# Kernel optimization log

Hardware: AMD Instinct MI355X
Metric: run time of the kernel (lower is better)

The kernel has to match this reference:

```python
import jax, jax.numpy as jnp
import numpy as np

# Output order of the stacked loss vector (7,):
# [loss_pose_intra_t, loss_pose_inter_t, loss_pose_intra_s, loss_pose_inter_s,
#  loss_pose_t, loss_pose_s, loss_pose]
ALPHA_T = 0.5
ALPHA_S = 0.75
ALPHA_TS = 0.5
EPS = 1e-8


def setup_inputs() -> dict:
    key = jax.random.key(0)
    k1, k2 = jax.random.split(key)
    B, M, C = 32, 784, 4
    pred_dT = jax.random.normal(k1, (B, M, M, C), dtype=jnp.float32)
    gt_dT = jax.random.normal(k2, (B, M, M, C), dtype=jnp.float32)
    # V=4 views, 196 tokens each; sum(Ms) must equal M
    Ms = jnp.full((4,), 196, dtype=jnp.int32)
    return {"pred_dT": pred_dT, "gt_dT": gt_dT, "Ms": Ms}


def reference(pred_dT, gt_dT, Ms):
    B, M, _, C = pred_dT.shape
    V = Ms.shape[0]
    dtype = pred_dT.dtype

    # criterion = 'mse', reduction='none'
    loss_full = (pred_dT - gt_dT) ** 2  # (B, M, M, C)

    # view id per token; same-view (intra) pair mask (M, M)
    view_ids = jnp.repeat(jnp.arange(V), Ms, total_repeat_length=M)
    intra_mask = (view_ids[:, None] == view_ids[None, :]).astype(dtype)

    # per-channel sums over all pairs and over intra-view pairs
    per_ch_all = loss_full.sum(axis=(0, 1, 2))                       # (C,)
    per_ch_intra = jnp.einsum('bijc,ij->c', loss_full, intra_mask)   # (C,)

    total_all_t = per_ch_all[0:2].sum()
    total_all_s = per_ch_all[2:4].sum()
    total_intra_t = per_ch_intra[0:2].sum()
    total_intra_s = per_ch_intra[2:4].sum()
    total_inter_t = total_all_t - total_intra_t
    total_inter_s = total_all_s - total_intra_s

    sum_Ms_sq = jnp.sum(Ms * Ms)
    diag_count = (sum_Ms_sq * B).astype(dtype)
    offdiag_count = ((M * M - sum_Ms_sq) * B).astype(dtype)

    zero = jnp.zeros((), dtype)
    loss_intra_t = jnp.where(diag_count > EPS, total_intra_t / diag_count, zero)
    loss_inter_t = jnp.where(offdiag_count > EPS, total_inter_t / offdiag_count, zero)
    loss_intra_s = jnp.where(diag_count > EPS, total_intra_s / diag_count, zero)
    loss_inter_s = jnp.where(offdiag_count > EPS, total_inter_s / offdiag_count, zero)

    loss_t = ALPHA_T * loss_inter_t + (1.0 - ALPHA_T) * loss_intra_t
    loss_s = ALPHA_S * loss_inter_s + (1.0 - ALPHA_S) * loss_intra_s
    loss = ALPHA_TS * loss_t + (1.0 - ALPHA_TS) * loss_s

    return jnp.stack([loss_intra_t, loss_inter_t, loss_intra_s, loss_inter_s,
                      loss_t, loss_s, loss])
```

## Files before the change

kernel.cpp:

```cpp
#include <hip/hip_runtime.h>

constexpr int B_ = 32;
constexpr int M_ = 784;
constexpr int C_ = 4;

constexpr int NBLK = 2048;
constexpr int NTHR = 256;

constexpr float ALPHA_T  = 0.5f;
constexpr float ALPHA_S  = 0.75f;
constexpr float ALPHA_TS = 0.5f;
constexpr float EPS      = 1e-8f;

__global__ __launch_bounds__(NTHR) void pose_loss_partial_kernel(
    const float* __restrict__ pred, const float* __restrict__ gt,
    const int* __restrict__ Ms, float4* __restrict__ partials)
{
    const int cum0 = Ms[0];
    const int cum1 = cum0 + Ms[1];
    const int cum2 = cum1 + Ms[2];

    float all_t = 0.f, all_s = 0.f, intra_t = 0.f, intra_s = 0.f;

    const int R = B_ * M_;
    for (int row = blockIdx.x; row < R; row += gridDim.x) {
        const int i  = row % M_;
        const int vi = (i >= cum0) + (i >= cum1) + (i >= cum2);
        const float4* __restrict__ prow =
            reinterpret_cast<const float4*>(pred + (size_t)row * (M_ * C_));
        const float4* __restrict__ grow =
            reinterpret_cast<const float4*>(gt   + (size_t)row * (M_ * C_));
        for (int j = threadIdx.x; j < M_; j += NTHR) {
            const float4 p = prow[j];
            const float4 g = grow[j];
            const float d0 = p.x - g.x;
            const float d1 = p.y - g.y;
            const float d2 = p.z - g.z;
            const float d3 = p.w - g.w;
            const float t = d0 * d0 + d1 * d1;
            const float s = d2 * d2 + d3 * d3;
            all_t += t;
            all_s += s;
            const int vj = (j >= cum0) + (j >= cum1) + (j >= cum2);
            if (vi == vj) { intra_t += t; intra_s += s; }
        }
    }

    float v0 = all_t, v1 = all_s, v2 = intra_t, v3 = intra_s;
    #pragma unroll
    for (int off = 32; off > 0; off >>= 1) {
        v0 += __shfl_down(v0, off, 64);
        v1 += __shfl_down(v1, off, 64);
        v2 += __shfl_down(v2, off, 64);
        v3 += __shfl_down(v3, off, 64);
    }

    __shared__ float4 sm[NTHR / 64];
    const int lane = threadIdx.x & 63;
    const int wid  = threadIdx.x >> 6;
    if (lane == 0) sm[wid] = make_float4(v0, v1, v2, v3);
    __syncthreads();

    if (threadIdx.x == 0) {
        float4 acc = sm[0];
        #pragma unroll
        for (int w = 1; w < NTHR / 64; ++w) {
            acc.x += sm[w].x; acc.y += sm[w].y;
            acc.z += sm[w].z; acc.w += sm[w].w;
        }
        partials[blockIdx.x] = acc;
    }
}

__global__ __launch_bounds__(NTHR) void pose_loss_final_kernel(
    const float4* __restrict__ partials, const int* __restrict__ Ms,
    float* __restrict__ out)
{
    float v0 = 0.f, v1 = 0.f, v2 = 0.f, v3 = 0.f;
    for (int p = threadIdx.x; p < NBLK; p += NTHR) {
        const float4 q = partials[p];
        v0 += q.x; v1 += q.y; v2 += q.z; v3 += q.w;
    }
    #pragma unroll
    for (int off = 32; off > 0; off >>= 1) {
        v0 += __shfl_down(v0, off, 64);
        v1 += __shfl_down(v1, off, 64);
        v2 += __shfl_down(v2, off, 64);
        v3 += __shfl_down(v3, off, 64);
    }
    __shared__ float4 sm[NTHR / 64];
    const int lane = threadIdx.x & 63;
    const int wid  = threadIdx.x >> 6;
    if (lane == 0) sm[wid] = make_float4(v0, v1, v2, v3);
    __syncthreads();

    if (threadIdx.x == 0) {
        float4 acc = sm[0];
        #pragma unroll
        for (int w = 1; w < NTHR / 64; ++w) {
            acc.x += sm[w].x; acc.y += sm[w].y;
            acc.z += sm[w].z; acc.w += sm[w].w;
        }
        const float total_all_t   = acc.x;
        const float total_all_s   = acc.y;
        const float total_intra_t = acc.z;
        const float total_intra_s = acc.w;
        const float total_inter_t = total_all_t - total_intra_t;
        const float total_inter_s = total_all_s - total_intra_s;

        int sum_Ms_sq = 0;
        #pragma unroll
        for (int v = 0; v < 4; ++v) sum_Ms_sq += Ms[v] * Ms[v];
        const float diag_count    = (float)((long long)sum_Ms_sq * B_);
        const float offdiag_count = (float)(((long long)M_ * M_ - sum_Ms_sq) * B_);

        const float li_t = (diag_count    > EPS) ? total_intra_t / diag_count    : 0.f;
        const float le_t = (offdiag_count > EPS) ? total_inter_t / offdiag_count : 0.f;
        const float li_s = (diag_count    > EPS) ? total_intra_s / diag_count    : 0.f;
        const float le_s = (offdiag_count > EPS) ? total_inter_s / offdiag_count : 0.f;

        const float loss_t = ALPHA_T  * le_t + (1.f - ALPHA_T)  * li_t;
        const float loss_s = ALPHA_S  * le_s + (1.f - ALPHA_S)  * li_s;
        const float loss   = ALPHA_TS * loss_t + (1.f - ALPHA_TS) * loss_s;

        out[0] = li_t;
        out[1] = le_t;
        out[2] = li_s;
        out[3] = le_s;
        out[4] = loss_t;
        out[5] = loss_s;
        out[6] = loss;
    }
}

extern "C" void kernel_launch(void* const* d_in, const int* in_sizes, int n_in,
                              void* d_out, int out_size, void* d_ws, size_t ws_size,
                              hipStream_t stream) {
    const float* pred = (const float*)d_in[0];
    const float* gt   = (const float*)d_in[1];
    const int*   Ms   = (const int*)d_in[2];
    float*       out  = (float*)d_out;
    float4*      partials = (float4*)d_ws;

    pose_loss_partial_kernel<<<NBLK, NTHR, 0, stream>>>(pred, gt, Ms, partials);
    pose_loss_final_kernel<<<1, NTHR, 0, stream>>>(partials, Ms, out);
}
```

Before: 117.5 us.

## Flatten reduction to grid-stride over elements with fixed trip count

Replaces the per-row loop, where 784 float4 per row left 256-thread blocks with a ragged 4th iteration (only 16 active lanes), with a flat grid-stride loop over all B*M*M float4 elements. The trip count is now a compile-time constant with one tail check, and the grid shrinks to 1792 blocks. This removes lane idling on the row tail and keeps memory requests uniform. The cost is recomputing row and column indices with integer divisions per element.

```diff
diff --git a/kernel.cpp b/kernel.cpp
--- a/kernel.cpp
+++ b/kernel.cpp
@@ -2,10 +2,12 @@
 
 constexpr int B_ = 32;
 constexpr int M_ = 784;
-constexpr int C_ = 4;
 
-constexpr int NBLK = 2048;
+constexpr int NBLK = 1792;
 constexpr int NTHR = 256;
+constexpr int TOTAL  = B_ * M_ * M_;
+constexpr int STRIDE = NBLK * NTHR;
+constexpr int KFULL  = TOTAL / STRIDE;
 
 constexpr float ALPHA_T  = 0.5f;
 constexpr float ALPHA_S  = 0.75f;
@@ -13,7 +15,7 @@
 constexpr float EPS      = 1e-8f;
 
 __global__ __launch_bounds__(NTHR) void pose_loss_partial_kernel(
-    const float* __restrict__ pred, const float* __restrict__ gt,
+    const float4* __restrict__ pred, const float4* __restrict__ gt,
     const int* __restrict__ Ms, float4* __restrict__ partials)
 {
     const int cum0 = Ms[0];
@@ -22,28 +24,32 @@
 
     float all_t = 0.f, all_s = 0.f, intra_t = 0.f, intra_s = 0.f;
 
-    const int R = B_ * M_;
-    for (int row = blockIdx.x; row < R; row += gridDim.x) {
-        const int i  = row % M_;
+    auto body = [&](int idx) {
+        const float4 p = pred[idx];
+        const float4 g = gt[idx];
+        const float d0 = p.x - g.x;
+        const float d1 = p.y - g.y;
+        const float d2 = p.z - g.z;
+        const float d3 = p.w - g.w;
+        const float t = d0 * d0 + d1 * d1;
+        const float s = d2 * d2 + d3 * d3;
+        all_t += t;
+        all_s += s;
+        const int q = idx / M_;
+        const int j = idx - q * M_;
+        const int i = q - (q / M_) * M_;
         const int vi = (i >= cum0) + (i >= cum1) + (i >= cum2);
-        const float4* __restrict__ prow =
-            reinterpret_cast<const float4*>(pred + (size_t)row * (M_ * C_));
-        const float4* __restrict__ grow =
-            reinterpret_cast<const float4*>(gt   + (size_t)row * (M_ * C_));
-        for (int j = threadIdx.x; j < M_; j += NTHR) {
-            const float4 p = prow[j];
-            const float4 g = grow[j];
-            const float d0 = p.x - g.x;
-            const float d1 = p.y - g.y;
-            const float d2 = p.z - g.z;
-            const float d3 = p.w - g.w;
-            const float t = d0 * d0 + d1 * d1;
-            const float s = d2 * d2 + d3 * d3;
-            all_t += t;
-            all_s += s;
-            const int vj = (j >= cum0) + (j >= cum1) + (j >= cum2);
-            if (vi == vj) { intra_t += t; intra_s += s; }
-        }
+        const int vj = (j >= cum0) + (j >= cum1) + (j >= cum2);
+        if (vi == vj) { intra_t += t; intra_s += s; }
+    };
+
+    int idx = blockIdx.x * NTHR + threadIdx.x;
+    #pragma unroll 2
+    for (int k = 0; k < KFULL; ++k, idx += STRIDE) {
+        body(idx);
+    }
+    if (idx < TOTAL) {
+        body(idx);
     }
 
     float v0 = all_t, v1 = all_s, v2 = intra_t, v3 = intra_s;
@@ -136,11 +142,11 @@
 extern "C" void kernel_launch(void* const* d_in, const int* in_sizes, int n_in,
                               void* d_out, int out_size, void* d_ws, size_t ws_size,
                               hipStream_t stream) {
-    const float* pred = (const float*)d_in[0];
-    const float* gt   = (const float*)d_in[1];
-    const int*   Ms   = (const int*)d_in[2];
-    float*       out  = (float*)d_out;
-    float4*      partials = (float4*)d_ws;
+    const float4* pred = (const float4*)d_in[0];
+    const float4* gt   = (const float4*)d_in[1];
+    const int*    Ms   = (const int*)d_in[2];
+    float*        out  = (float*)d_out;
+    float4*       partials = (float4*)d_ws;
 
     pose_loss_partial_kernel<<<NBLK, NTHR, 0, stream>>>(pred, gt, Ms, partials);
     pose_loss_final_kernel<<<1, NTHR, 0, stream>>>(partials, Ms, out);
```

Result: faster. 113.0 us (-3.8%).
